# Kernel tuning notes

Measured on AMD Instinct MI355X. Metric: run time of the kernel, lower is better.

The kernel has to match this reference:

```python
import jax, jax.numpy as jnp
import numpy as np

SCALE_H = 160.0
SCALE_W = 160.0
ALIGNED = False


def setup_inputs() -> dict:
    key = jax.random.key(0)
    k1, k2, k3, k4 = jax.random.split(key, 4)
    N, C, H, W, K = 8, 256, 160, 160, 1024
    feat = jax.random.normal(k1, (N, C, H, W), dtype=jnp.float32)
    b = jax.random.randint(k2, (K,), 0, N).astype(jnp.float32)
    xs = jnp.sort(jax.random.uniform(k3, (K, 2), dtype=jnp.float32), axis=1)
    ys = jnp.sort(jax.random.uniform(k4, (K, 2), dtype=jnp.float32), axis=1)
    rois = jnp.stack([b, xs[:, 0], ys[:, 0], xs[:, 1], ys[:, 1]], axis=1)
    return {"input_feature_map": feat, "rois": rois,
            "output_height": 14, "output_width": 14}


def _roi_align(feat, rois, output_height, output_width):
    N, C, H, W = feat.shape
    K = rois.shape[0]
    b = rois[:, 0].astype(jnp.int32)
    x1 = rois[:, 1] * SCALE_W
    y1 = rois[:, 2] * SCALE_H
    x2 = rois[:, 3] * SCALE_W
    y2 = rois[:, 4] * SCALE_H
    # normalized [0,1] grid over the ROI interior
    gx = jnp.linspace(0.0, 1.0, output_width, dtype=feat.dtype)
    gy = jnp.linspace(0.0, 1.0, output_height, dtype=feat.dtype)
    fx = x1[:, None, None] + gx[None, None, :] * (x2 - x1)[:, None, None]  # (K,1,Wo)
    fy = y1[:, None, None] + gy[None, :, None] * (y2 - y1)[:, None, None]  # (K,Ho,1)
    # convert to grid_sample normalized coords, then back to pixel coords
    if ALIGNED:
        ngx = fx / (W - 1) * 2 - 1
        ngy = fy / (H - 1) * 2 - 1
        ix = (ngx + 1) * 0.5 * (W - 1)
        iy = (ngy + 1) * 0.5 * (H - 1)
    else:
        ngx = fx / W * 2 - 1
        ngy = fy / H * 2 - 1
        ix = ((ngx + 1) * W - 1) * 0.5
        iy = ((ngy + 1) * H - 1) * 0.5
    x0 = jnp.floor(ix).astype(jnp.int32)
    y0 = jnp.floor(iy).astype(jnp.int32)
    x1i = x0 + 1
    y1i = y0 + 1
    wx1 = ix - x0.astype(feat.dtype)
    wx0 = 1.0 - wx1
    wy1 = iy - y0.astype(feat.dtype)
    wy0 = 1.0 - wy1
    # zeros padding: out-of-bounds corners contribute 0
    vx0 = ((x0 >= 0) & (x0 < W)).astype(feat.dtype)
    vx1 = ((x1i >= 0) & (x1i < W)).astype(feat.dtype)
    vy0 = ((y0 >= 0) & (y0 < H)).astype(feat.dtype)
    vy1 = ((y1i >= 0) & (y1i < H)).astype(feat.dtype)
    x0c = jnp.clip(x0, 0, W - 1)
    x1c = jnp.clip(x1i, 0, W - 1)
    y0c = jnp.clip(y0, 0, H - 1)
    y1c = jnp.clip(y1i, 0, H - 1)
    # flat gather table: (N*H*W, C) -- no per-ROI feature-map duplication
    featf = jnp.transpose(feat, (0, 2, 3, 1)).reshape(N * H * W, C)
    bb = b[:, None, None]  # (K,1,1)

    def corner(yy, xx, w):
        lin = (bb * H + yy) * W + xx  # broadcast -> (K,Ho,Wo)
        lin = jnp.broadcast_to(lin, (K, output_height, output_width))
        v = featf[lin.reshape(-1)].reshape(K, output_height, output_width, C)
        w = jnp.broadcast_to(w, (K, output_height, output_width))
        return v * w[..., None]

    out = (corner(y0c, x0c, wy0 * wx0 * vy0 * vx0)
           + corner(y0c, x1c, wy0 * wx1 * vy0 * vx1)
           + corner(y1c, x0c, wy1 * wx0 * vy1 * vx0)
           + corner(y1c, x1c, wy1 * wx1 * vy1 * vx1))
    return jnp.transpose(out, (0, 3, 1, 2))  # (K, C, Ho, Wo)


def reference(input_feature_map, rois, output_height, output_width):
    return _roi_align(input_feature_map, rois, int(output_height), int(output_width))
```

## Files before the change

kernel.cpp:

```cpp
#include <hip/hip_runtime.h>
#include <hip/hip_fp16.h>


#define FM_N 8
#define FM_C 256
#define FM_H 160
#define FM_W 160
#define PLANE (FM_H * FM_W)
#define PLANE4 (PLANE / 4)
#define OH 14
#define OW 14
#define OSP (OH * OW)
#define KMAX 1024
#define SCALE_HW 160.0f
#define MAIN_BLK 1024
#define NCP 2
#define STG_IT 7

typedef float f4 __attribute__((ext_vector_type(4)));

#define WS_KLIST_OFF 16
#define WS_SAMPLES_BYTE_OFF 4224

__global__ void setup_kernel(const float* __restrict__ rois, int K,
                             int* __restrict__ ws) {
  __shared__ int cnt[FM_N];
  __shared__ int koff[FM_N];
  const int t = threadIdx.x;
  if (t < FM_N) cnt[t] = 0;
  __syncthreads();
  int myb = -1, pos = 0;
  if (t < K) {
    myb = (int)rois[t * 5];
    pos = atomicAdd(&cnt[myb], 1);
  }
  __syncthreads();
  if (t == 0) {
    int acc = 0;
    for (int b = 0; b < FM_N; ++b) { koff[b] = acc; acc += cnt[b]; }
  }
  __syncthreads();
  if (t < K) ws[WS_KLIST_OFF + koff[myb] + pos] = t;
  if (t < FM_N) { ws[t] = cnt[t]; ws[FM_N + t] = koff[t]; }
}

__global__ __launch_bounds__(256) void precompute_kernel(
    const float* __restrict__ rois, const int* __restrict__ ws, int K,
    uint2* __restrict__ samples) {
  const int g = blockIdx.x * 256 + threadIdx.x;
  if (g >= K * OSP) return;
  const int slot = g / OSP;
  const int s = g - slot * OSP;
  const int k = ws[WS_KLIST_OFF + slot];

  const float x1 = rois[k * 5 + 1] * SCALE_HW;
  const float y1 = rois[k * 5 + 2] * SCALE_HW;
  const float x2 = rois[k * 5 + 3] * SCALE_HW;
  const float y2 = rois[k * 5 + 4] * SCALE_HW;

  const int oy = s / OW;
  const int ox = s - oy * OW;
  const float gx = (float)ox * (1.0f / (OW - 1));
  const float gy = (float)oy * (1.0f / (OH - 1));

  const float ix = x1 + gx * (x2 - x1) - 0.5f;
  const float iy = y1 + gy * (y2 - y1) - 0.5f;

  const float fx0 = floorf(ix);
  const float fy0 = floorf(iy);
  const int x0 = (int)fx0;
  const int y0 = (int)fy0;
  const float wx1 = ix - fx0;
  const float wy1 = iy - fy0;

  const bool vx0 = (x0 >= 0 && x0 < FM_W);
  const bool vx1 = (x0 + 1 >= 0 && x0 + 1 < FM_W);
  const unsigned vy0 = (y0 >= 0 && y0 < FM_H) ? 1u : 0u;
  const unsigned vy1 = (y0 + 1 >= 0 && y0 + 1 < FM_H) ? 1u : 0u;

  const int x0c = min(max(x0, 0), FM_W - 1);
  const int x1c = min(max(x0 + 1, 0), FM_W - 1);
  const int y0c = min(max(y0, 0), FM_H - 1);
  const int y1c = min(max(y0 + 1, 0), FM_H - 1);

  const int o00 = y0c * FM_W + x0c;
  const int o01 = y0c * FM_W + x1c;
  const int bx = vx1 ? (o01 - 1) : o00;
  const unsigned bxs = (unsigned)(bx + 4);
  const unsigned dyr = (unsigned)(y1c - y0c);
  unsigned wq = (unsigned)(wy1 * 8192.0f + 0.5f);
  wq = wq > 8191u ? 8191u : wq;

  const __half2 axh = __floats2half2_rn((1.0f - wx1) * (vx0 ? 1.0f : 0.0f),
                                        wx1 * (vx1 ? 1.0f : 0.0f));

  uint2 sd;
  sd.x = bxs | (dyr << 15) | (wq << 16) | (vy0 << 29) | (vy1 << 30);
  sd.y = *(const unsigned*)&axh;
  samples[(size_t)slot * OSP + s] = sd;
}

__global__ __launch_bounds__(MAIN_BLK) void roi_align_main_kernel(
    const float* __restrict__ feat, const int* __restrict__ ws,
    const uint2* __restrict__ samples, float* __restrict__ out) {
  __shared__ __align__(16) __half2 planeBuf[PLANE + 8];
  __shared__ int klist[KMAX];

  const int b = blockIdx.y;
  const int p0 = blockIdx.x * NCP;
  const int t = threadIdx.x;

  const int cnt = ws[b];
  const int koff = ws[FM_N + b];
  for (int i = t; i < cnt; i += MAIN_BLK)
    klist[i] = ws[WS_KLIST_OFF + koff + i] * (FM_C * OSP);
  if (t < 4) {
    planeBuf[t] = __floats2half2_rn(0.0f, 0.0f);
    planeBuf[PLANE + 4 + t] = __floats2half2_rn(0.0f, 0.0f);
  }

  const uint2* __restrict__ sam = samples + (size_t)koff * OSP;
  const int total = cnt * OSP;
  const f4* __restrict__ fbase = (const f4*)feat + (size_t)b * FM_C * PLANE4;
  __half2* __restrict__ planeP = planeBuf + 4;

  f4 ra[STG_IT], rb[STG_IT];

  auto load_pair = [&](int p) {
    const f4* __restrict__ srcA = fbase + (size_t)(2 * p) * PLANE4;
    const f4* __restrict__ srcB = srcA + PLANE4;
#pragma unroll
    for (int i = 0; i < STG_IT; ++i) {
      const int idx = t + i * MAIN_BLK;
      if (idx < PLANE4) {
        ra[i] = __builtin_nontemporal_load(&srcA[idx]);
        rb[i] = __builtin_nontemporal_load(&srcB[idx]);
      }
    }
  };

  auto write_plane = [&]() {
    uint4* __restrict__ pl4 = (uint4*)planeP;
#pragma unroll
    for (int i = 0; i < STG_IT; ++i) {
      const int idx = t + i * MAIN_BLK;
      if (idx < PLANE4) {
        const __half2 h0 = __floats2half2_rn(ra[i].x, rb[i].x);
        const __half2 h1 = __floats2half2_rn(ra[i].y, rb[i].y);
        const __half2 h2 = __floats2half2_rn(ra[i].z, rb[i].z);
        const __half2 h3 = __floats2half2_rn(ra[i].w, rb[i].w);
        uint4 u;
        u.x = *(const unsigned*)&h0;
        u.y = *(const unsigned*)&h1;
        u.z = *(const unsigned*)&h2;
        u.w = *(const unsigned*)&h3;
        pl4[idx] = u;
      }
    }
  };

  auto compute_pair = [&](int c0) {
    float* __restrict__ outc = out + (size_t)c0 * OSP;
#pragma unroll 4
    for (int w = t; w < total; w += MAIN_BLK) {
      const uint2 sd = sam[w];
      const unsigned kl = (unsigned)w / OSP;
      const int s = w - (int)kl * OSP;
      const int kbase = klist[kl];

      const int bxs = (int)(sd.x & 0x7FFFu);
      const int b2 = bxs + (int)((sd.x >> 15) & 1u) * FM_W;

      const __half2 pL0 = planeP[bxs - 4];
      const __half2 pR0 = planeP[bxs - 3];
      const __half2 pL1 = planeP[b2 - 4];
      const __half2 pR1 = planeP[b2 - 3];

      const __half2 ax = *(const __half2*)&sd.y;
      const __half2 axl = __half2half2(__low2half(ax));
      const __half2 axr = __half2half2(__high2half(ax));
      const __half2 hx0 = __hfma2(pR0, axr, __hmul2(pL0, axl));
      const __half2 hx1 = __hfma2(pR1, axr, __hmul2(pL1, axl));

      const float wy1 = (float)((sd.x >> 16) & 0x1FFFu) * (1.0f / 8192.0f);
      const float ay0 = ((sd.x >> 29) & 1u) ? (1.0f - wy1) : 0.0f;
      const float ay1 = ((sd.x >> 30) & 1u) ? wy1 : 0.0f;

      const float vA = ay0 * __low2float(hx0) + ay1 * __low2float(hx1);
      const float vB = ay0 * __high2float(hx0) + ay1 * __high2float(hx1);

      const size_t ob = (size_t)(kbase + s);
      outc[ob] = vA;
      outc[ob + OSP] = vB;
    }
  };

  load_pair(p0);
  write_plane();
  __syncthreads();

  for (int cp = 0; cp < NCP; ++cp) {
    if (cp + 1 < NCP) load_pair(p0 + cp + 1);
    compute_pair(2 * (p0 + cp));
    if (cp + 1 < NCP) {
      __syncthreads();
      write_plane();
      __syncthreads();
    }
  }
}

extern "C" void kernel_launch(void* const* d_in, const int* in_sizes, int n_in,
                              void* d_out, int out_size, void* d_ws, size_t ws_size,
                              hipStream_t stream) {
  const float* feat = (const float*)d_in[0];
  const float* rois = (const float*)d_in[1];
  float* out = (float*)d_out;
  int* ws = (int*)d_ws;
  uint2* samples = (uint2*)((char*)d_ws + WS_SAMPLES_BYTE_OFF);

  const int K = in_sizes[1] / 5;

  setup_kernel<<<1, 1024, 0, stream>>>(rois, K, ws);
  precompute_kernel<<<(K * OSP + 255) / 256, 256, 0, stream>>>(rois, ws, K,
                                                               samples);
  roi_align_main_kernel<<<dim3(FM_C / 2 / NCP, FM_N), MAIN_BLK, 0, stream>>>(
      feat, ws, samples, out);
}
```

Baseline: 98.74 us.

## Split feature planes into half-height tiles with per-sample bucketed streams

Each sample is now bucketed by batch and by which half of the feature map its top row falls in, using a count/prefix/place pass. The main kernel stages only 81 rows of a channel pair into LDS, which roughly halves shared memory. That allows more resident blocks with 512 threads each and a z-dimension of 2 blocks per batch. Samples now carry a precomputed output offset, so the klist lookup and the division go away. The cost is roughly redundant feature loads for the overlapping row, and the two extra setup kernels plus a memset add launch overhead.

New measurement: 161.3 us. 1.63x slower.

```diff
diff --git a/kernel.cpp b/kernel.cpp
--- a/kernel.cpp
+++ b/kernel.cpp
@@ -11,170 +11,184 @@
 #define OH 14
 #define OW 14
 #define OSP (OH * OW)
-#define KMAX 1024
+#define KTOT (1024 * OSP)
 #define SCALE_HW 160.0f
-#define MAIN_BLK 1024
+#define MAIN_BLK 512
 #define NCP 2
-#define STG_IT 7
+#define ROWS 81
+#define PL_ENT (ROWS * FM_W)
+#define PL_F4 (PL_ENT / 4)
 
 typedef float f4 __attribute__((ext_vector_type(4)));
 
-#define WS_KLIST_OFF 16
-#define WS_SAMPLES_BYTE_OFF 4224
-
-__global__ void setup_kernel(const float* __restrict__ rois, int K,
-                             int* __restrict__ ws) {
-  __shared__ int cnt[FM_N];
-  __shared__ int koff[FM_N];
+#define WS_SAMPLES_BYTE_OFF 256
+
+__global__ __launch_bounds__(256) void pass1_count(
+    const float* __restrict__ rois, int total, int* __restrict__ ws) {
+  __shared__ int hist[16];
   const int t = threadIdx.x;
-  if (t < FM_N) cnt[t] = 0;
-  __syncthreads();
-  int myb = -1, pos = 0;
-  if (t < K) {
-    myb = (int)rois[t * 5];
-    pos = atomicAdd(&cnt[myb], 1);
-  }
-  __syncthreads();
-  if (t == 0) {
+  if (t < 16) hist[t] = 0;
+  __syncthreads();
+  const int g = blockIdx.x * 256 + t;
+  if (g < total) {
+    const int k = g / OSP;
+    const int s = g - k * OSP;
+    const int oy = s / OW;
+    const int b = (int)rois[k * 5];
+    const float y1 = rois[k * 5 + 2] * SCALE_HW;
+    const float y2 = rois[k * 5 + 4] * SCALE_HW;
+    const float gy = (float)oy * (1.0f / (OH - 1));
+    const float iy = y1 + gy * (y2 - y1) - 0.5f;
+    const int y0 = (int)floorf(iy);
+    const int y0c = min(max(y0, 0), FM_H - 1);
+    const int h = (y0c >= 80) ? 1 : 0;
+    atomicAdd(&hist[b * 2 + h], 1);
+  }
+  __syncthreads();
+  if (t < 16 && hist[t]) atomicAdd(&ws[t], hist[t]);
+}
+
+__global__ void prefix16(int* __restrict__ ws) {
+  if (threadIdx.x == 0) {
     int acc = 0;
-    for (int b = 0; b < FM_N; ++b) { koff[b] = acc; acc += cnt[b]; }
-  }
-  __syncthreads();
-  if (t < K) ws[WS_KLIST_OFF + koff[myb] + pos] = t;
-  if (t < FM_N) { ws[t] = cnt[t]; ws[FM_N + t] = koff[t]; }
-}
-
-__global__ __launch_bounds__(256) void precompute_kernel(
-    const float* __restrict__ rois, const int* __restrict__ ws, int K,
-    uint2* __restrict__ samples) {
-  const int g = blockIdx.x * 256 + threadIdx.x;
-  if (g >= K * OSP) return;
-  const int slot = g / OSP;
-  const int s = g - slot * OSP;
-  const int k = ws[WS_KLIST_OFF + slot];
-
-  const float x1 = rois[k * 5 + 1] * SCALE_HW;
-  const float y1 = rois[k * 5 + 2] * SCALE_HW;
-  const float x2 = rois[k * 5 + 3] * SCALE_HW;
-  const float y2 = rois[k * 5 + 4] * SCALE_HW;
-
-  const int oy = s / OW;
-  const int ox = s - oy * OW;
-  const float gx = (float)ox * (1.0f / (OW - 1));
-  const float gy = (float)oy * (1.0f / (OH - 1));
-
-  const float ix = x1 + gx * (x2 - x1) - 0.5f;
-  const float iy = y1 + gy * (y2 - y1) - 0.5f;
-
-  const float fx0 = floorf(ix);
-  const float fy0 = floorf(iy);
-  const int x0 = (int)fx0;
-  const int y0 = (int)fy0;
-  const float wx1 = ix - fx0;
-  const float wy1 = iy - fy0;
-
-  const bool vx0 = (x0 >= 0 && x0 < FM_W);
-  const bool vx1 = (x0 + 1 >= 0 && x0 + 1 < FM_W);
-  const unsigned vy0 = (y0 >= 0 && y0 < FM_H) ? 1u : 0u;
-  const unsigned vy1 = (y0 + 1 >= 0 && y0 + 1 < FM_H) ? 1u : 0u;
-
-  const int x0c = min(max(x0, 0), FM_W - 1);
-  const int x1c = min(max(x0 + 1, 0), FM_W - 1);
-  const int y0c = min(max(y0, 0), FM_H - 1);
-  const int y1c = min(max(y0 + 1, 0), FM_H - 1);
-
-  const int o00 = y0c * FM_W + x0c;
-  const int o01 = y0c * FM_W + x1c;
-  const int bx = vx1 ? (o01 - 1) : o00;
-  const unsigned bxs = (unsigned)(bx + 4);
-  const unsigned dyr = (unsigned)(y1c - y0c);
-  unsigned wq = (unsigned)(wy1 * 8192.0f + 0.5f);
-  wq = wq > 8191u ? 8191u : wq;
-
-  const __half2 axh = __floats2half2_rn((1.0f - wx1) * (vx0 ? 1.0f : 0.0f),
-                                        wx1 * (vx1 ? 1.0f : 0.0f));
-
-  uint2 sd;
-  sd.x = bxs | (dyr << 15) | (wq << 16) | (vy0 << 29) | (vy1 << 30);
-  sd.y = *(const unsigned*)&axh;
-  samples[(size_t)slot * OSP + s] = sd;
-}
-
-__global__ __launch_bounds__(MAIN_BLK) void roi_align_main_kernel(
+    for (int i = 0; i < 16; ++i) {
+      ws[16 + i] = acc;
+      acc += ws[i];
+      ws[32 + i] = 0;
+    }
+  }
+}
+
+__global__ __launch_bounds__(256) void pass2_place(
+    const float* __restrict__ rois, int total, int* __restrict__ ws,
+    uint4* __restrict__ samples) {
+  __shared__ int hist[16];
+  __shared__ int basel[16];
+  __shared__ int soffl[16];
+  const int t = threadIdx.x;
+  if (t < 16) hist[t] = 0;
+  __syncthreads();
+
+  const int g = blockIdx.x * 256 + t;
+  const bool act = g < total;
+  uint4 sd = {0, 0, 0, 0};
+  int bh = 0;
+  if (act) {
+    const int k = g / OSP;
+    const int s = g - k * OSP;
+    const int b = (int)rois[k * 5];
+    const float x1 = rois[k * 5 + 1] * SCALE_HW;
+    const float y1 = rois[k * 5 + 2] * SCALE_HW;
+    const float x2 = rois[k * 5 + 3] * SCALE_HW;
+    const float y2 = rois[k * 5 + 4] * SCALE_HW;
+
+    const int oy = s / OW;
+    const int ox = s - oy * OW;
+    const float gx = (float)ox * (1.0f / (OW - 1));
+    const float gy = (float)oy * (1.0f / (OH - 1));
+
+    const float ix = x1 + gx * (x2 - x1) - 0.5f;
+    const float iy = y1 + gy * (y2 - y1) - 0.5f;
+
+    const float fx0 = floorf(ix);
+    const float fy0 = floorf(iy);
+    const int x0 = (int)fx0;
+    const int y0 = (int)fy0;
+    const float wx1 = ix - fx0;
+    const float wy1 = iy - fy0;
+
+    const bool vx0 = (x0 >= 0 && x0 < FM_W);
+    const bool vx1 = (x0 + 1 >= 0 && x0 + 1 < FM_W);
+    const unsigned vy0 = (y0 >= 0 && y0 < FM_H) ? 1u : 0u;
+    const unsigned vy1 = (y0 + 1 >= 0 && y0 + 1 < FM_H) ? 1u : 0u;
+
+    const int x0c = min(max(x0, 0), FM_W - 1);
+    const int x1c = min(max(x0 + 1, 0), FM_W - 1);
+    const int y0c = min(max(y0, 0), FM_H - 1);
+    const int y1c = min(max(y0 + 1, 0), FM_H - 1);
+
+    const int o00 = y0c * FM_W + x0c;
+    const int o01 = y0c * FM_W + x1c;
+    const int bx = vx1 ? (o01 - 1) : o00;
+    const int h = (y0c >= 80) ? 1 : 0;
+    const int row0 = h ? 79 : 0;
+    const unsigned bxs = (unsigned)(bx - row0 * FM_W + 4);
+    const unsigned dyr = (unsigned)(y1c - y0c);
+    unsigned wq = (unsigned)(wy1 * 8192.0f + 0.5f);
+    wq = wq > 8191u ? 8191u : wq;
+
+    const __half2 axh = __floats2half2_rn((1.0f - wx1) * (vx0 ? 1.0f : 0.0f),
+                                          wx1 * (vx1 ? 1.0f : 0.0f));
+    sd.x = bxs | (dyr << 15) | (wq << 16) | (vy0 << 29) | (vy1 << 30);
+    sd.y = *(const unsigned*)&axh;
+    sd.z = (unsigned)(k * (FM_C * OSP) + s);
+    bh = b * 2 + h;
+  }
+  const int rank = act ? atomicAdd(&hist[bh], 1) : 0;
+  __syncthreads();
+  if (t < 16) {
+    basel[t] = hist[t] ? atomicAdd(&ws[32 + t], hist[t]) : 0;
+    soffl[t] = ws[16 + t];
+  }
+  __syncthreads();
+  if (act) samples[(size_t)soffl[bh] + basel[bh] + rank] = sd;
+}
+
+__global__ __launch_bounds__(MAIN_BLK, 4) void roi_align_main_kernel(
     const float* __restrict__ feat, const int* __restrict__ ws,
-    const uint2* __restrict__ samples, float* __restrict__ out) {
-  __shared__ __align__(16) __half2 planeBuf[PLANE + 8];
-  __shared__ int klist[KMAX];
-
+    const uint4* __restrict__ samples, float* __restrict__ out) {
+  __shared__ __align__(16) __half2 planeBuf[PL_ENT + 8];
+
+  const int pg = blockIdx.x;
   const int b = blockIdx.y;
-  const int p0 = blockIdx.x * NCP;
+  const int h = blockIdx.z;
   const int t = threadIdx.x;
-
-  const int cnt = ws[b];
-  const int koff = ws[FM_N + b];
-  for (int i = t; i < cnt; i += MAIN_BLK)
-    klist[i] = ws[WS_KLIST_OFF + koff + i] * (FM_C * OSP);
+  const int row0 = h ? 79 : 0;
+
+  const int scount = ws[b * 2 + h];
+  const int soff = ws[16 + b * 2 + h];
+  const uint4* __restrict__ stream = samples + soff;
+
   if (t < 4) {
     planeBuf[t] = __floats2half2_rn(0.0f, 0.0f);
-    planeBuf[PLANE + 4 + t] = __floats2half2_rn(0.0f, 0.0f);
-  }
-
-  const uint2* __restrict__ sam = samples + (size_t)koff * OSP;
-  const int total = cnt * OSP;
-  const f4* __restrict__ fbase = (const f4*)feat + (size_t)b * FM_C * PLANE4;
-  __half2* __restrict__ planeP = planeBuf + 4;
-
-  f4 ra[STG_IT], rb[STG_IT];
-
-  auto load_pair = [&](int p) {
-    const f4* __restrict__ srcA = fbase + (size_t)(2 * p) * PLANE4;
+    planeBuf[4 + PL_ENT + t] = __floats2half2_rn(0.0f, 0.0f);
+  }
+
+  for (int cp = 0; cp < NCP; ++cp) {
+    const int c0 = 2 * (pg * NCP + cp);
+    if (cp) __syncthreads();
+
+    const f4* __restrict__ srcA =
+        (const f4*)(feat + ((size_t)b * FM_C + c0) * PLANE) + row0 * (FM_W / 4);
     const f4* __restrict__ srcB = srcA + PLANE4;
-#pragma unroll
-    for (int i = 0; i < STG_IT; ++i) {
-      const int idx = t + i * MAIN_BLK;
-      if (idx < PLANE4) {
-        ra[i] = __builtin_nontemporal_load(&srcA[idx]);
-        rb[i] = __builtin_nontemporal_load(&srcB[idx]);
-      }
+    uint4* __restrict__ pl4 = (uint4*)(planeBuf + 4);
+    for (int i = t; i < PL_F4; i += MAIN_BLK) {
+      const f4 a = srcA[i];
+      const f4 bb = srcB[i];
+      const __half2 h0 = __floats2half2_rn(a.x, bb.x);
+      const __half2 h1 = __floats2half2_rn(a.y, bb.y);
+      const __half2 h2 = __floats2half2_rn(a.z, bb.z);
+      const __half2 h3 = __floats2half2_rn(a.w, bb.w);
+      uint4 u;
+      u.x = *(const unsigned*)&h0;
+      u.y = *(const unsigned*)&h1;
+      u.z = *(const unsigned*)&h2;
+      u.w = *(const unsigned*)&h3;
+      pl4[i] = u;
     }
-  };
-
-  auto write_plane = [&]() {
-    uint4* __restrict__ pl4 = (uint4*)planeP;
-#pragma unroll
-    for (int i = 0; i < STG_IT; ++i) {
-      const int idx = t + i * MAIN_BLK;
-      if (idx < PLANE4) {
-        const __half2 h0 = __floats2half2_rn(ra[i].x, rb[i].x);
-        const __half2 h1 = __floats2half2_rn(ra[i].y, rb[i].y);
-        const __half2 h2 = __floats2half2_rn(ra[i].z, rb[i].z);
-        const __half2 h3 = __floats2half2_rn(ra[i].w, rb[i].w);
-        uint4 u;
-        u.x = *(const unsigned*)&h0;
-        u.y = *(const unsigned*)&h1;
-        u.z = *(const unsigned*)&h2;
-        u.w = *(const unsigned*)&h3;
-        pl4[idx] = u;
-      }
-    }
-  };
-
-  auto compute_pair = [&](int c0) {
+    __syncthreads();
+
     float* __restrict__ outc = out + (size_t)c0 * OSP;
-#pragma unroll 4
-    for (int w = t; w < total; w += MAIN_BLK) {
-      const uint2 sd = sam[w];
-      const unsigned kl = (unsigned)w / OSP;
-      const int s = w - (int)kl * OSP;
-      const int kbase = klist[kl];
-
+#pragma unroll 2
+    for (int w = t; w < scount; w += MAIN_BLK) {
+      const uint4 sd = stream[w];
       const int bxs = (int)(sd.x & 0x7FFFu);
-      const int b2 = bxs + (int)((sd.x >> 15) & 1u) * FM_W;
-
-      const __half2 pL0 = planeP[bxs - 4];
-      const __half2 pR0 = planeP[bxs - 3];
-      const __half2 pL1 = planeP[b2 - 4];
-      const __half2 pR1 = planeP[b2 - 3];
+      const int o10 = bxs + (int)((sd.x >> 15) & 1u) * FM_W;
+
+      const __half2 pL0 = planeBuf[bxs];
+      const __half2 pR0 = planeBuf[bxs + 1];
+      const __half2 pL1 = planeBuf[o10];
+      const __half2 pR1 = planeBuf[o10 + 1];
 
       const __half2 ax = *(const __half2*)&sd.y;
       const __half2 axl = __half2half2(__low2half(ax));
@@ -189,23 +203,9 @@
       const float vA = ay0 * __low2float(hx0) + ay1 * __low2float(hx1);
       const float vB = ay0 * __high2float(hx0) + ay1 * __high2float(hx1);
 
-      const size_t ob = (size_t)(kbase + s);
-      outc[ob] = vA;
-      outc[ob + OSP] = vB;
-    }
-  };
-
-  load_pair(p0);
-  write_plane();
-  __syncthreads();
-
-  for (int cp = 0; cp < NCP; ++cp) {
-    if (cp + 1 < NCP) load_pair(p0 + cp + 1);
-    compute_pair(2 * (p0 + cp));
-    if (cp + 1 < NCP) {
-      __syncthreads();
-      write_plane();
-      __syncthreads();
+      float* __restrict__ dst = outc + sd.z;
+      dst[0] = vA;
+      dst[OSP] = vB;
     }
   }
 }
@@ -217,13 +217,16 @@
   const float* rois = (const float*)d_in[1];
   float* out = (float*)d_out;
   int* ws = (int*)d_ws;
-  uint2* samples = (uint2*)((char*)d_ws + WS_SAMPLES_BYTE_OFF);
+  uint4* samples = (uint4*)((char*)d_ws + WS_SAMPLES_BYTE_OFF);
 
   const int K = in_sizes[1] / 5;
-
-  setup_kernel<<<1, 1024, 0, stream>>>(rois, K, ws);
-  precompute_kernel<<<(K * OSP + 255) / 256, 256, 0, stream>>>(rois, ws, K,
-                                                               samples);
-  roi_align_main_kernel<<<dim3(FM_C / 2 / NCP, FM_N), MAIN_BLK, 0, stream>>>(
+  const int total = K * OSP;
+  const int nblk = (total + 255) / 256;
+
+  hipMemsetAsync(d_ws, 0, 64, stream);
+  pass1_count<<<nblk, 256, 0, stream>>>(rois, total, ws);
+  prefix16<<<1, 64, 0, stream>>>(ws);
+  pass2_place<<<nblk, 256, 0, stream>>>(rois, total, ws, samples);
+  roi_align_main_kernel<<<dim3(FM_C / 2 / NCP, FM_N, 2), MAIN_BLK, 0, stream>>>(
       feat, ws, samples, out);
 }
```

## Pad LDS plane rows to stride 164 and drop register prefetch pipelining

Applied to the files above, without the earlier changes.

Stores the fp16 channel-pair plane in LDS with a padded row stride of 164 entries, zeroing the pad columns, and updates the precomputed sample offsets to match. The intent is to reduce LDS bank conflicts on bilinear gathers. It also removes the software pipeline that prefetched the next channel pair into registers during compute, replacing it with a simple load-convert-store loop. This lowers register pressure but gives up overlap of global loads with compute.

Measured after the change: 121.2 us. 1.23x slower.

```diff
diff --git a/kernel.cpp b/kernel.cpp
--- a/kernel.cpp
+++ b/kernel.cpp
@@ -8,6 +8,9 @@
 #define FM_W 160
 #define PLANE (FM_H * FM_W)
 #define PLANE4 (PLANE / 4)
+#define LDSW 164
+#define LROW4 (LDSW / 4)
+#define PL_ENT (FM_H * LDSW)
 #define OH 14
 #define OW 14
 #define OSP (OH * OW)
@@ -15,7 +18,8 @@
 #define SCALE_HW 160.0f
 #define MAIN_BLK 1024
 #define NCP 2
-#define STG_IT 7
+#define FRONTPAD 4
+#define TAILPAD 8
 
 typedef float f4 __attribute__((ext_vector_type(4)));
 
@@ -83,17 +87,16 @@
   const int y0c = min(max(y0, 0), FM_H - 1);
   const int y1c = min(max(y0 + 1, 0), FM_H - 1);
 
-  const int o00 = y0c * FM_W + x0c;
-  const int o01 = y0c * FM_W + x1c;
+  const int o00 = y0c * LDSW + x0c;
+  const int o01 = y0c * LDSW + x1c;
   const int bx = vx1 ? (o01 - 1) : o00;
-  const unsigned bxs = (unsigned)(bx + 4);
+  const unsigned bxs = (unsigned)(bx + FRONTPAD);
   const unsigned dyr = (unsigned)(y1c - y0c);
   unsigned wq = (unsigned)(wy1 * 8192.0f + 0.5f);
   wq = wq > 8191u ? 8191u : wq;
 
   const __half2 axh = __floats2half2_rn((1.0f - wx1) * (vx0 ? 1.0f : 0.0f),
                                         wx1 * (vx1 ? 1.0f : 0.0f));
-
   uint2 sd;
   sd.x = bxs | (dyr << 15) | (wq << 16) | (vy0 << 29) | (vy1 << 30);
   sd.y = *(const unsigned*)&axh;
@@ -103,7 +106,7 @@
 __global__ __launch_bounds__(MAIN_BLK) void roi_align_main_kernel(
     const float* __restrict__ feat, const int* __restrict__ ws,
     const uint2* __restrict__ samples, float* __restrict__ out) {
-  __shared__ __align__(16) __half2 planeBuf[PLANE + 8];
+  __shared__ __align__(16) __half2 planeBuf[FRONTPAD + PL_ENT + TAILPAD];
   __shared__ int klist[KMAX];
 
   const int b = blockIdx.y;
@@ -114,52 +117,44 @@
   const int koff = ws[FM_N + b];
   for (int i = t; i < cnt; i += MAIN_BLK)
     klist[i] = ws[WS_KLIST_OFF + koff + i] * (FM_C * OSP);
-  if (t < 4) {
-    planeBuf[t] = __floats2half2_rn(0.0f, 0.0f);
-    planeBuf[PLANE + 4 + t] = __floats2half2_rn(0.0f, 0.0f);
+
+  const __half2 hz = __floats2half2_rn(0.0f, 0.0f);
+  if (t < FRONTPAD) planeBuf[t] = hz;
+  if (t < TAILPAD) planeBuf[FRONTPAD + PL_ENT + t] = hz;
+  if (t < FM_H * 4) {
+    const int y = t >> 2;
+    planeBuf[FRONTPAD + y * LDSW + FM_W + (t & 3)] = hz;
   }
 
   const uint2* __restrict__ sam = samples + (size_t)koff * OSP;
   const int total = cnt * OSP;
-  const f4* __restrict__ fbase = (const f4*)feat + (size_t)b * FM_C * PLANE4;
-  __half2* __restrict__ planeP = planeBuf + 4;
-
-  f4 ra[STG_IT], rb[STG_IT];
-
-  auto load_pair = [&](int p) {
-    const f4* __restrict__ srcA = fbase + (size_t)(2 * p) * PLANE4;
+
+  for (int cp = 0; cp < NCP; ++cp) {
+    const int c0 = 2 * (p0 + cp);
+    if (cp) __syncthreads();
+
+    const f4* __restrict__ srcA =
+        (const f4*)(feat + ((size_t)b * FM_C + c0) * PLANE);
     const f4* __restrict__ srcB = srcA + PLANE4;
-#pragma unroll
-    for (int i = 0; i < STG_IT; ++i) {
-      const int idx = t + i * MAIN_BLK;
-      if (idx < PLANE4) {
-        ra[i] = __builtin_nontemporal_load(&srcA[idx]);
-        rb[i] = __builtin_nontemporal_load(&srcB[idx]);
-      }
+    uint4* __restrict__ pl4 = (uint4*)(planeBuf + FRONTPAD);
+    for (int i = t; i < PLANE4; i += MAIN_BLK) {
+      const f4 a = srcA[i];
+      const f4 bb = srcB[i];
+      const int y = i / (FM_W / 4);
+      const int j = i - y * (FM_W / 4);
+      const __half2 h0 = __floats2half2_rn(a.x, bb.x);
+      const __half2 h1 = __floats2half2_rn(a.y, bb.y);
+      const __half2 h2 = __floats2half2_rn(a.z, bb.z);
+      const __half2 h3 = __floats2half2_rn(a.w, bb.w);
+      uint4 u;
+      u.x = *(const unsigned*)&h0;
+      u.y = *(const unsigned*)&h1;
+      u.z = *(const unsigned*)&h2;
+      u.w = *(const unsigned*)&h3;
+      pl4[y * LROW4 + j] = u;
     }
-  };
-
-  auto write_plane = [&]() {
-    uint4* __restrict__ pl4 = (uint4*)planeP;
-#pragma unroll
-    for (int i = 0; i < STG_IT; ++i) {
-      const int idx = t + i * MAIN_BLK;
-      if (idx < PLANE4) {
-        const __half2 h0 = __floats2half2_rn(ra[i].x, rb[i].x);
-        const __half2 h1 = __floats2half2_rn(ra[i].y, rb[i].y);
-        const __half2 h2 = __floats2half2_rn(ra[i].z, rb[i].z);
-        const __half2 h3 = __floats2half2_rn(ra[i].w, rb[i].w);
-        uint4 u;
-        u.x = *(const unsigned*)&h0;
-        u.y = *(const unsigned*)&h1;
-        u.z = *(const unsigned*)&h2;
-        u.w = *(const unsigned*)&h3;
-        pl4[idx] = u;
-      }
-    }
-  };
-
-  auto compute_pair = [&](int c0) {
+    __syncthreads();
+
     float* __restrict__ outc = out + (size_t)c0 * OSP;
 #pragma unroll 4
     for (int w = t; w < total; w += MAIN_BLK) {
@@ -169,12 +164,12 @@
       const int kbase = klist[kl];
 
       const int bxs = (int)(sd.x & 0x7FFFu);
-      const int b2 = bxs + (int)((sd.x >> 15) & 1u) * FM_W;
-
-      const __half2 pL0 = planeP[bxs - 4];
-      const __half2 pR0 = planeP[bxs - 3];
-      const __half2 pL1 = planeP[b2 - 4];
-      const __half2 pR1 = planeP[b2 - 3];
+      const int o10 = bxs + (int)((sd.x >> 15) & 1u) * LDSW;
+
+      const __half2 pL0 = planeBuf[bxs];
+      const __half2 pR0 = planeBuf[bxs + 1];
+      const __half2 pL1 = planeBuf[o10];
+      const __half2 pR1 = planeBuf[o10 + 1];
 
       const __half2 ax = *(const __half2*)&sd.y;
       const __half2 axl = __half2half2(__low2half(ax));
@@ -192,20 +187,6 @@
       const size_t ob = (size_t)(kbase + s);
       outc[ob] = vA;
       outc[ob + OSP] = vB;
-    }
-  };
-
-  load_pair(p0);
-  write_plane();
-  __syncthreads();
-
-  for (int cp = 0; cp < NCP; ++cp) {
-    if (cp + 1 < NCP) load_pair(p0 + cp + 1);
-    compute_pair(2 * (p0 + cp));
-    if (cp + 1 < NCP) {
-      __syncthreads();
-      write_plane();
-      __syncthreads();
     }
   }
 }
```
